# Kernel tuning notes

Measured on AMD Instinct MI355X. Metric: run time of the kernel, lower is better.

The kernel has to match this reference:

```python
import jax, jax.numpy as jnp
import numpy as np

B, T, C, E, K = 4, 4096, 2048, 64, 8


def setup_inputs() -> dict:
    key = jax.random.key(0)
    k1, k2, k3 = jax.random.split(key, 3)
    hidden_states = jax.random.normal(k1, (B, T, C), dtype=jnp.float32)
    mask = jax.random.randint(k2, (B, T), 0, 2).astype(bool)
    gate_weight = jax.random.normal(k3, (E, C), dtype=jnp.float32) * 0.02
    gate_bias = jnp.zeros((E,), dtype=jnp.float32)
    expert_biases = jnp.zeros((E,), dtype=jnp.float32)
    return {
        "hidden_states": hidden_states,
        "mask": mask,
        "gate_weight": gate_weight,
        "gate_bias": gate_bias,
        "expert_biases": expert_biases,
    }


def reference(hidden_states, mask, gate_weight, gate_bias, expert_biases):
    Bc, Tc, Cc = hidden_states.shape
    n_experts = gate_weight.shape[0]
    x = hidden_states.reshape(-1, Cc)                 # [N, C]
    m = mask.reshape(-1)                              # [N]
    gate_output = x @ gate_weight.T + gate_bias       # [N, E]
    gate_probs = jax.nn.sigmoid(gate_output)
    gate_logits = gate_output + expert_biases
    _, top_k_indices = jax.lax.top_k(gate_logits, K)  # [N, K]
    top_k_probs = jnp.take_along_axis(gate_probs, top_k_indices, axis=-1)
    top_k_probs = top_k_probs / jnp.sum(top_k_probs, axis=-1, keepdims=True)
    # masked bincount of routed experts (only tokens where mask is True)
    weights = jnp.broadcast_to(m[:, None], top_k_indices.shape).astype(jnp.float32)
    expert_counts = jnp.zeros((n_experts,), jnp.float32).at[top_k_indices.reshape(-1)].add(weights.reshape(-1))
    avg_count = expert_counts.mean()
    maxvio = (expert_counts.max() - avg_count) / (avg_count + 1e-5)
    # note: the in-place expert_biases sign-update is a training-time, no-grad
    # side effect and does not change the returned values of this call.
    return top_k_indices, top_k_probs, maxvio
```

## Files before the change

kernel.cpp:

```cpp
#include <hip/hip_runtime.h>
#include <math.h>

#define NTOK   16384
#define CDIM   2048
#define NEXP   64
#define TOPK   8
#define GBLK   256

typedef _Float16 f16x8 __attribute__((ext_vector_type(8)));
typedef float    f32x4 __attribute__((ext_vector_type(4)));

__global__ __launch_bounds__(256) void pack_w16_kernel(
    const float* __restrict__ W,
    _Float16* __restrict__ Wh, _Float16* __restrict__ Wl)
{
    int t    = blockIdx.x * 256 + threadIdx.x;
    int lane = t & 63;
    int nt   = (t >> 6) & 3;
    int s    = t >> 8;
    int e    = nt * 16 + (lane & 15);
    int k    = s * 32 + (lane >> 4) * 8;
    const float* src = W + (size_t)e * CDIM + k;
    #pragma unroll
    for (int j = 0; j < 8; j++) {
        float x = src[j];
        _Float16 h = (_Float16)x;
        Wh[(size_t)t * 8 + j] = h;
        Wl[(size_t)t * 8 + j] = (_Float16)(x - (float)h);
    }
}

__device__ __forceinline__ void mfma_step(
    const float4 v0, const float4 v1,
    const f16x8* __restrict__ bh, const f16x8* __restrict__ bl,
    f32x4* __restrict__ acc)
{
    float xr[8] = {v0.x, v0.y, v0.z, v0.w, v1.x, v1.y, v1.z, v1.w};
    f16x8 ah, al;
    #pragma unroll
    for (int j = 0; j < 8; j++) {
        _Float16 h = (_Float16)xr[j];
        ah[j] = h;
        al[j] = (_Float16)(xr[j] - (float)h);
    }
    #pragma unroll
    for (int nt = 0; nt < 4; nt++) {
        acc[nt] = __builtin_amdgcn_mfma_f32_16x16x32_f16(ah, bh[nt], acc[nt], 0, 0, 0);
        acc[nt] = __builtin_amdgcn_mfma_f32_16x16x32_f16(al, bh[nt], acc[nt], 0, 0, 0);
        acc[nt] = __builtin_amdgcn_mfma_f32_16x16x32_f16(ah, bl[nt], acc[nt], 0, 0, 0);
    }
}

__global__ __launch_bounds__(256, 4) void gate_fused_kernel(
    const float* __restrict__ x,
    const _Float16* __restrict__ Wh,
    const _Float16* __restrict__ Wl,
    const int*   __restrict__ mask,
    const float* __restrict__ gbias,
    const float* __restrict__ ebias,
    float*       __restrict__ out,
    float*       __restrict__ blockcnt)
{
    __shared__ unsigned int cnt[NEXP];
    const int tid  = threadIdx.x;
    const int lane = tid & 63;
    const int wid  = tid >> 6;
    if (tid < NEXP) cnt[tid] = 0u;
    __syncthreads();

    const int tok0 = blockIdx.x * 64 + wid * 16;
    const int col  = lane & 15;
    const int q    = lane >> 4;
    const float* xp = x + (size_t)(tok0 + col) * CDIM + q * 8;
    const f16x8* bhp = (const f16x8*)Wh + lane;
    const f16x8* blp = (const f16x8*)Wl + lane;

    f32x4 acc[4];
    #pragma unroll
    for (int nt = 0; nt < 4; nt++) acc[nt] = (f32x4){0.f, 0.f, 0.f, 0.f};

    float4 a0v0, a0v1, a1v0, a1v1;
    f16x8 b0h[4], b0l[4], b1h[4], b1l[4];

    a0v0 = *(const float4*)(xp);
    a0v1 = *(const float4*)(xp + 4);
    #pragma unroll
    for (int nt = 0; nt < 4; nt++) { b0h[nt] = bhp[nt * 64]; b0l[nt] = blp[nt * 64]; }

    for (int s = 0; s < 64; s += 2) {
        a1v0 = *(const float4*)(xp + (s + 1) * 32);
        a1v1 = *(const float4*)(xp + (s + 1) * 32 + 4);
        #pragma unroll
        for (int nt = 0; nt < 4; nt++) {
            b1h[nt] = bhp[(s + 1) * 256 + nt * 64];
            b1l[nt] = blp[(s + 1) * 256 + nt * 64];
        }
        mfma_step(a0v0, a0v1, b0h, b0l, acc);

        const int s2 = (s + 2 < 64) ? (s + 2) : 63;
        a0v0 = *(const float4*)(xp + s2 * 32);
        a0v1 = *(const float4*)(xp + s2 * 32 + 4);
        #pragma unroll
        for (int nt = 0; nt < 4; nt++) {
            b0h[nt] = bhp[s2 * 256 + nt * 64];
            b0l[nt] = blp[s2 * 256 + nt * 64];
        }
        mfma_step(a1v0, a1v1, b1h, b1l, acc);
    }

    float gb[4], eb[4];
    #pragma unroll
    for (int nt = 0; nt < 4; nt++) {
        gb[nt] = gbias[nt * 16 + col];
        eb[nt] = ebias[nt * 16 + col];
    }

    #pragma unroll
    for (int r = 0; r < 4; r++) {
        const int t = tok0 + q * 4 + r;
        float z[4], sel[4];
        #pragma unroll
        for (int nt = 0; nt < 4; nt++) {
            z[nt]   = acc[nt][r] + gb[nt];
            sel[nt] = z[nt] + eb[nt];
        }

        int idxs[TOPK]; float probs[TOPK]; float psum = 0.f;
        #pragma unroll
        for (int rr = 0; rr < TOPK; rr++) {
            float bv = -INFINITY, bz = 0.f; int bidx = 1 << 30;
            #pragma unroll
            for (int nt = 0; nt < 4; nt++)
                if (sel[nt] > bv) { bv = sel[nt]; bz = z[nt]; bidx = nt * 16 + col; }
            #pragma unroll
            for (int m = 1; m < 16; m <<= 1) {
                float ov = __shfl_xor(bv, m);
                float oz = __shfl_xor(bz, m);
                int   oi = __shfl_xor(bidx, m);
                if (ov > bv || (ov == bv && oi < bidx)) { bv = ov; bz = oz; bidx = oi; }
            }
            idxs[rr] = bidx;
            float p = 1.f / (1.f + expf(-bz));
            probs[rr] = p; psum += p;
            if ((bidx & 15) == col) sel[bidx >> 4] = -INFINITY;
        }
        float inv = 1.f / psum;
        if (col < TOPK) {
            out[(size_t)t * TOPK + col] = (float)idxs[col];
            out[(size_t)NTOK * TOPK + (size_t)t * TOPK + col] = probs[col] * inv;
            if (mask[t] != 0) atomicAdd(&cnt[idxs[col]], 1u);
        }
    }
    __syncthreads();
    if (tid < NEXP)
        blockcnt[(size_t)blockIdx.x * NEXP + tid] = (float)cnt[tid];
}

__global__ __launch_bounds__(256) void finalize_kernel(
    const float* __restrict__ blockcnt, float* __restrict__ out)
{
    __shared__ float ps[4][NEXP];
    const int t = threadIdx.x;
    const int e = t & 63, c = t >> 6;
    float s = 0.f;
    #pragma unroll 8
    for (int b = 0; b < GBLK / 4; b++)
        s += blockcnt[(size_t)(c * (GBLK / 4) + b) * NEXP + e];
    ps[c][e] = s;
    __syncthreads();
    if (t < 64) {
        float tot = ps[0][t] + ps[1][t] + ps[2][t] + ps[3][t];
        float mx = tot, sm = tot;
        #pragma unroll
        for (int o = 32; o > 0; o >>= 1) {
            mx = fmaxf(mx, __shfl_down(mx, o));
            sm += __shfl_down(sm, o);
        }
        if (t == 0) {
            float avg = sm / (float)NEXP;
            out[2 * NTOK * TOPK] = (mx - avg) / (avg + 1e-5f);
        }
    }
}

__global__ __launch_bounds__(256) void fused_fallback_kernel(
    const float* __restrict__ x, const int* __restrict__ mask,
    const float* __restrict__ W, const float* __restrict__ gbias,
    const float* __restrict__ ebias, float* __restrict__ out,
    unsigned int* __restrict__ counts)
{
    __shared__ float As[64][36];
    __shared__ float Bs[64][36];
    __shared__ float Lg[64][NEXP + 1];
    __shared__ float s_gb[NEXP], s_eb[NEXP];
    __shared__ unsigned int s_cnt[NEXP];
    const int tid = threadIdx.x;
    const int tx = tid & 15, ty = tid >> 4;
    const int m0 = blockIdx.x * 64;
    if (tid < NEXP) { s_gb[tid] = gbias[tid]; s_eb[tid] = ebias[tid]; s_cnt[tid] = 0u; }
    float acc[4][4] = {};
    for (int kb = 0; kb < CDIM; kb += 32) {
        __syncthreads();
        #pragma unroll
        for (int p = 0; p < 2; p++) {
            int lin = tid + p * 256; int m = lin >> 3; int c4 = (lin & 7) << 2;
            *(float4*)&As[m][c4] = *(const float4*)&x[(size_t)(m0 + m) * CDIM + kb + c4];
            *(float4*)&Bs[m][c4] = *(const float4*)&W[(size_t)m * CDIM + kb + c4];
        }
        __syncthreads();
        #pragma unroll
        for (int k4 = 0; k4 < 32; k4 += 4) {
            float4 a[4], b[4];
            #pragma unroll
            for (int i = 0; i < 4; i++) a[i] = *(const float4*)&As[ty * 4 + i][k4];
            #pragma unroll
            for (int j = 0; j < 4; j++) b[j] = *(const float4*)&Bs[tx * 4 + j][k4];
            #pragma unroll
            for (int i = 0; i < 4; i++)
                #pragma unroll
                for (int j = 0; j < 4; j++)
                    acc[i][j] += a[i].x * b[j].x + a[i].y * b[j].y
                               + a[i].z * b[j].z + a[i].w * b[j].w;
        }
    }
    __syncthreads();
    #pragma unroll
    for (int i = 0; i < 4; i++)
        #pragma unroll
        for (int j = 0; j < 4; j++)
            Lg[ty * 4 + i][tx * 4 + j] = acc[i][j] + s_gb[tx * 4 + j];
    __syncthreads();
    if (tid < 64) {
        const int g = m0 + tid;
        unsigned long long used = 0ull;
        int idxs[TOPK]; float probs[TOPK]; float psum = 0.f;
        #pragma unroll
        for (int k = 0; k < TOPK; k++) {
            float best = -INFINITY; int bi = 0;
            for (int n = 0; n < NEXP; n++) {
                if ((used >> n) & 1ull) continue;
                float vv = Lg[tid][n] + s_eb[n];
                if (vv > best) { best = vv; bi = n; }
            }
            used |= (1ull << bi);
            idxs[k] = bi;
            float p = 1.f / (1.f + expf(-Lg[tid][bi]));
            probs[k] = p; psum += p;
        }
        float inv = 1.f / psum;
        #pragma unroll
        for (int k = 0; k < TOPK; k++) {
            out[(size_t)g * TOPK + k] = (float)idxs[k];
            out[(size_t)NTOK * TOPK + (size_t)g * TOPK + k] = probs[k] * inv;
        }
        if (mask[g] != 0)
            #pragma unroll
            for (int k = 0; k < TOPK; k++) atomicAdd(&s_cnt[idxs[k]], 1u);
    }
    __syncthreads();
    if (tid < NEXP && s_cnt[tid] != 0u) atomicAdd(&counts[tid], s_cnt[tid]);
}

__global__ void finalize_atomic_kernel(const unsigned int* __restrict__ counts,
                                       float* __restrict__ out)
{
    const int t = threadIdx.x;
    float c  = (float)counts[t];
    float mx = c, sm = c;
    #pragma unroll
    for (int o = 32; o > 0; o >>= 1) {
        mx = fmaxf(mx, __shfl_down(mx, o));
        sm += __shfl_down(sm, o);
    }
    if (t == 0) {
        float avg = sm / (float)NEXP;
        out[2 * NTOK * TOPK] = (mx - avg) / (avg + 1e-5f);
    }
}

extern "C" void kernel_launch(void* const* d_in, const int* in_sizes, int n_in,
                              void* d_out, int out_size, void* d_ws, size_t ws_size,
                              hipStream_t stream)
{
    const float* x     = (const float*)d_in[0];
    const int*   mask  = (const int*)  d_in[1];
    const float* W     = (const float*)d_in[2];
    const float* gbias = (const float*)d_in[3];
    const float* ebias = (const float*)d_in[4];
    float* out = (float*)d_out;

    const size_t whB  = (size_t)NEXP * CDIM * sizeof(_Float16);
    const size_t bcB  = (size_t)GBLK * NEXP * sizeof(float);
    const size_t need = 2 * whB + bcB;

    if (ws_size >= need) {
        _Float16* Wh = (_Float16*)d_ws;
        _Float16* Wl = (_Float16*)((char*)d_ws + whB);
        float* blockcnt = (float*)((char*)d_ws + 2 * whB);

        pack_w16_kernel<<<64, 256, 0, stream>>>(W, Wh, Wl);
        gate_fused_kernel<<<GBLK, 256, 0, stream>>>(x, Wh, Wl, mask, gbias, ebias, out, blockcnt);
        finalize_kernel<<<1, 256, 0, stream>>>(blockcnt, out);
        return;
    }

    unsigned int* counts = (unsigned int*)d_ws;
    hipMemsetAsync(d_ws, 0, NEXP * sizeof(unsigned int), stream);
    fused_fallback_kernel<<<NTOK / 64, 256, 0, stream>>>(x, mask, W, gbias, ebias, out, counts);
    finalize_atomic_kernel<<<1, 64, 0, stream>>>(counts, out);
}
```

Before: 270.1 us.

## Split K dimension across waves with shared-memory reduction of gate logits

Each block now handles 16 tokens instead of 64, and its four waves each compute a quarter of the C reduction, combining partial accumulators through shared memory before wave 0 does the top-k. The grid grows from 256 to 1024 blocks to expose more parallelism and better fill the GPU's compute units. In exchange it adds an LDS reduction and a barrier, drops the explicit double-buffered prefetch, leaves three waves idle during the top-k epilogue, and makes finalize read four times as many block counts.

After: 239.5 us. 1.13x faster.

```diff
diff --git a/kernel.cpp b/kernel.cpp
--- a/kernel.cpp
+++ b/kernel.cpp
@@ -5,7 +5,7 @@
 #define CDIM   2048
 #define NEXP   64
 #define TOPK   8
-#define GBLK   256
+#define GBLK   1024
 
 typedef _Float16 f16x8 __attribute__((ext_vector_type(8)));
 typedef float    f32x4 __attribute__((ext_vector_type(4)));
@@ -61,99 +61,93 @@
     float*       __restrict__ out,
     float*       __restrict__ blockcnt)
 {
+    __shared__ f32x4 sacc[4][64][4];
     __shared__ unsigned int cnt[NEXP];
     const int tid  = threadIdx.x;
     const int lane = tid & 63;
     const int wid  = tid >> 6;
     if (tid < NEXP) cnt[tid] = 0u;
-    __syncthreads();
-
-    const int tok0 = blockIdx.x * 64 + wid * 16;
+
+    const int tok0 = blockIdx.x * 16;
     const int col  = lane & 15;
     const int q    = lane >> 4;
-    const float* xp = x + (size_t)(tok0 + col) * CDIM + q * 8;
-    const f16x8* bhp = (const f16x8*)Wh + lane;
-    const f16x8* blp = (const f16x8*)Wl + lane;
+    const float* xp = x + (size_t)(tok0 + col) * CDIM + wid * 512 + q * 8;
+    const f16x8* bhp = (const f16x8*)Wh + (size_t)wid * 16 * 256 + lane;
+    const f16x8* blp = (const f16x8*)Wl + (size_t)wid * 16 * 256 + lane;
 
     f32x4 acc[4];
     #pragma unroll
     for (int nt = 0; nt < 4; nt++) acc[nt] = (f32x4){0.f, 0.f, 0.f, 0.f};
 
-    float4 a0v0, a0v1, a1v0, a1v1;
-    f16x8 b0h[4], b0l[4], b1h[4], b1l[4];
-
-    a0v0 = *(const float4*)(xp);
-    a0v1 = *(const float4*)(xp + 4);
-    #pragma unroll
-    for (int nt = 0; nt < 4; nt++) { b0h[nt] = bhp[nt * 64]; b0l[nt] = blp[nt * 64]; }
-
-    for (int s = 0; s < 64; s += 2) {
-        a1v0 = *(const float4*)(xp + (s + 1) * 32);
-        a1v1 = *(const float4*)(xp + (s + 1) * 32 + 4);
+    #pragma unroll 2
+    for (int s = 0; s < 16; s++) {
+        float4 v0 = *(const float4*)(xp + s * 32);
+        float4 v1 = *(const float4*)(xp + s * 32 + 4);
+        f16x8 bh[4], bl[4];
         #pragma unroll
         for (int nt = 0; nt < 4; nt++) {
-            b1h[nt] = bhp[(s + 1) * 256 + nt * 64];
-            b1l[nt] = blp[(s + 1) * 256 + nt * 64];
-        }
-        mfma_step(a0v0, a0v1, b0h, b0l, acc);
-
-        const int s2 = (s + 2 < 64) ? (s + 2) : 63;
-        a0v0 = *(const float4*)(xp + s2 * 32);
-        a0v1 = *(const float4*)(xp + s2 * 32 + 4);
+            bh[nt] = bhp[s * 256 + nt * 64];
+            bl[nt] = blp[s * 256 + nt * 64];
+        }
+        mfma_step(v0, v1, bh, bl, acc);
+    }
+
+    #pragma unroll
+    for (int nt = 0; nt < 4; nt++) sacc[wid][lane][nt] = acc[nt];
+    __syncthreads();
+
+    if (wid == 0) {
+        f32x4 zv[4];
+        #pragma unroll
+        for (int nt = 0; nt < 4; nt++)
+            zv[nt] = sacc[0][lane][nt] + sacc[1][lane][nt]
+                   + sacc[2][lane][nt] + sacc[3][lane][nt];
+
+        float gb[4], eb[4];
         #pragma unroll
         for (int nt = 0; nt < 4; nt++) {
-            b0h[nt] = bhp[s2 * 256 + nt * 64];
-            b0l[nt] = blp[s2 * 256 + nt * 64];
-        }
-        mfma_step(a1v0, a1v1, b1h, b1l, acc);
-    }
-
-    float gb[4], eb[4];
-    #pragma unroll
-    for (int nt = 0; nt < 4; nt++) {
-        gb[nt] = gbias[nt * 16 + col];
-        eb[nt] = ebias[nt * 16 + col];
-    }
-
-    #pragma unroll
-    for (int r = 0; r < 4; r++) {
-        const int t = tok0 + q * 4 + r;
-        float z[4], sel[4];
-        #pragma unroll
-        for (int nt = 0; nt < 4; nt++) {
-            z[nt]   = acc[nt][r] + gb[nt];
-            sel[nt] = z[nt] + eb[nt];
-        }
-
-        int idxs[TOPK]; float probs[TOPK]; float psum = 0.f;
-        #pragma unroll
-        for (int rr = 0; rr < TOPK; rr++) {
-            float bv = -INFINITY, bz = 0.f; int bidx = 1 << 30;
-            #pragma unroll
-            for (int nt = 0; nt < 4; nt++)
-                if (sel[nt] > bv) { bv = sel[nt]; bz = z[nt]; bidx = nt * 16 + col; }
-            #pragma unroll
-            for (int m = 1; m < 16; m <<= 1) {
-                float ov = __shfl_xor(bv, m);
-                float oz = __shfl_xor(bz, m);
-                int   oi = __shfl_xor(bidx, m);
-                if (ov > bv || (ov == bv && oi < bidx)) { bv = ov; bz = oz; bidx = oi; }
+            gb[nt] = gbias[nt * 16 + col];
+            eb[nt] = ebias[nt * 16 + col];
+        }
+
+        #pragma unroll
+        for (int r = 0; r < 4; r++) {
+            const int t = tok0 + q * 4 + r;
+            float z[4], sel[4];
+            #pragma unroll
+            for (int nt = 0; nt < 4; nt++) {
+                z[nt]   = zv[nt][r] + gb[nt];
+                sel[nt] = z[nt] + eb[nt];
             }
-            idxs[rr] = bidx;
-            float p = 1.f / (1.f + expf(-bz));
-            probs[rr] = p; psum += p;
-            if ((bidx & 15) == col) sel[bidx >> 4] = -INFINITY;
-        }
-        float inv = 1.f / psum;
-        if (col < TOPK) {
-            out[(size_t)t * TOPK + col] = (float)idxs[col];
-            out[(size_t)NTOK * TOPK + (size_t)t * TOPK + col] = probs[col] * inv;
-            if (mask[t] != 0) atomicAdd(&cnt[idxs[col]], 1u);
-        }
-    }
-    __syncthreads();
-    if (tid < NEXP)
-        blockcnt[(size_t)blockIdx.x * NEXP + tid] = (float)cnt[tid];
+
+            int idxs[TOPK]; float probs[TOPK]; float psum = 0.f;
+            #pragma unroll
+            for (int rr = 0; rr < TOPK; rr++) {
+                float bv = -INFINITY, bz = 0.f; int bidx = 1 << 30;
+                #pragma unroll
+                for (int nt = 0; nt < 4; nt++)
+                    if (sel[nt] > bv) { bv = sel[nt]; bz = z[nt]; bidx = nt * 16 + col; }
+                #pragma unroll
+                for (int m = 1; m < 16; m <<= 1) {
+                    float ov = __shfl_xor(bv, m);
+                    float oz = __shfl_xor(bz, m);
+                    int   oi = __shfl_xor(bidx, m);
+                    if (ov > bv || (ov == bv && oi < bidx)) { bv = ov; bz = oz; bidx = oi; }
+                }
+                idxs[rr] = bidx;
+                float p = 1.f / (1.f + expf(-bz));
+                probs[rr] = p; psum += p;
+                if ((bidx & 15) == col) sel[bidx >> 4] = -INFINITY;
+            }
+            float inv = 1.f / psum;
+            if (col < TOPK) {
+                out[(size_t)t * TOPK + col] = (float)idxs[col];
+                out[(size_t)NTOK * TOPK + (size_t)t * TOPK + col] = probs[col] * inv;
+                if (mask[t] != 0) atomicAdd(&cnt[idxs[col]], 1u);
+            }
+        }
+        blockcnt[(size_t)blockIdx.x * NEXP + lane] = (float)cnt[lane];
+    }
 }
 
 __global__ __launch_bounds__(256) void finalize_kernel(
```
